# Optimization experiments

Measured on AMD Instinct MI355X. Metric: run time of the kernel, lower is better.

The kernel has to match this reference:

```python
import jax, jax.numpy as jnp
import numpy as np

NQ = 10
C64 = jnp.complex64

# ---- gate matrices (built from traced fp32 params) ----

def u3(t, p, d):
    c = jnp.cos(t * 0.5).astype(C64)
    s = jnp.sin(t * 0.5).astype(C64)
    ep = jnp.exp(1j * p.astype(C64))
    ed = jnp.exp(1j * d.astype(C64))
    return jnp.stack([jnp.stack([c, -ed * s]), jnp.stack([ep * s, ep * ed * c])])

def ry(t):
    c = jnp.cos(t * 0.5).astype(C64)
    s = jnp.sin(t * 0.5).astype(C64)
    return jnp.stack([jnp.stack([c, -s]), jnp.stack([s, c])])

def rz(t):
    e = jnp.exp(-0.5j * t.astype(C64))
    ep = jnp.exp(0.5j * t.astype(C64))
    return jnp.diag(jnp.stack([e, ep]))

def rx(t):
    c = jnp.cos(t * 0.5).astype(C64)
    s = jnp.sin(t * 0.5).astype(C64)
    return jnp.stack([jnp.stack([c, -1j * s]), jnp.stack([-1j * s, c])])

def crz(t):
    one = jnp.ones((), C64)
    return jnp.diag(jnp.stack([one, one, jnp.exp(-0.5j * t.astype(C64)), jnp.exp(0.5j * t.astype(C64))]))

def crx(t):
    return jnp.eye(4, dtype=C64).at[2:, 2:].set(rx(t))

X = jnp.array([[0, 1], [1, 0]], dtype=C64)
CNOT = jnp.array([[1, 0, 0, 0], [0, 1, 0, 0], [0, 0, 0, 1], [0, 0, 1, 0]], dtype=C64)

# ---- gate application on state of shape (B, 2,...,2) ----

def ap1(st, U, w):
    ax = 1 + w
    s = jnp.moveaxis(st, ax, -1)
    s = s @ U.T
    return jnp.moveaxis(s, -1, ax)

def ap2(st, U, a, b):
    s = jnp.moveaxis(st, (1 + a, 1 + b), (-2, -1))
    sh = s.shape
    s = s.reshape(sh[:-2] + (4,)) @ U.T
    return jnp.moveaxis(s.reshape(sh), (-2, -1), (1 + a, 1 + b))

def conv_block(st, w, a, b):
    st = ap1(st, u3(w[0], w[1], w[2]), a)
    st = ap1(st, u3(w[3], w[4], w[5]), b)
    st = ap2(st, CNOT, a, b)
    st = ap1(st, ry(w[6]), a)
    st = ap1(st, rz(w[7]), b)
    st = ap2(st, CNOT, b, a)
    st = ap1(st, ry(w[8]), a)
    st = ap2(st, CNOT, a, b)
    st = ap1(st, u3(w[9], w[10], w[11]), a)
    st = ap1(st, u3(w[12], w[13], w[14]), b)
    return st

def pool_block(st, p, c, t):
    st = ap2(st, crz(p[0]), c, t)
    st = ap1(st, X, c)
    st = ap2(st, crx(p[1]), c, t)
    return st

def zexp(st, w):
    p = jnp.abs(st) ** 2  # fp32
    axes = tuple(ax for ax in range(1, NQ + 1) if ax != 1 + w)
    pz = p.sum(axis=axes)  # (B, 2)
    return pz[:, 0] - pz[:, 1]


def setup_inputs() -> dict:
    key = jax.random.key(0)
    ks = jax.random.split(key, 6)
    two_pi = 2.0 * np.pi
    return {
        "x": jax.random.normal(ks[0], (16384, 1024), dtype=jnp.float32),
        "weights_conv1": jax.random.uniform(ks[1], (10, 15), jnp.float32) * two_pi,
        "weights_conv2": jax.random.uniform(ks[2], (4, 15), jnp.float32) * two_pi,
        "weights_pool1": jax.random.uniform(ks[3], (5, 2), jnp.float32) * two_pi,
        "weights_pool2": jax.random.uniform(ks[4], (2, 2), jnp.float32) * two_pi,
        "weights_fc": jax.random.uniform(ks[5], (3,), jnp.float32) * two_pi,
    }


def reference(x, weights_conv1, weights_conv2, weights_pool1, weights_pool2, weights_fc):
    B = x.shape[0]
    # AmplitudeEmbedding with normalize=True (input already 1024-dim, no padding)
    nrm = jnp.linalg.norm(x, axis=1, keepdims=True)
    st = (x / nrm).astype(C64).reshape((B,) + (2,) * NQ)
    # conv layer 1: even pairs, odd pairs, wraparound (0, 9) reusing row 7
    for i in range(0, NQ, 2):
        st = conv_block(st, weights_conv1[i], i, i + 1)
    for i in range(1, NQ - 1, 2):
        st = conv_block(st, weights_conv1[i], i, i + 1)
    st = conv_block(st, weights_conv1[7], 0, NQ - 1)
    # pool layer 1
    for idx, i in enumerate(range(0, NQ, 2)):
        st = pool_block(st, weights_pool1[idx], i + 1, i)
    # conv layer 2 (stride-2 wires)
    for idx, i in enumerate(range(0, NQ - 2, 2)):
        st = conv_block(st, weights_conv2[idx], i, i + 2)
    # pool layer 2
    for idx, i in enumerate(range(0, NQ - 2, 4)):
        st = pool_block(st, weights_pool2[idx], i + 2, i)
    # fully-connected entanglers + RX rotations
    st = ap2(st, CNOT, 0, 4)
    st = ap2(st, CNOT, 2, 4)
    st = ap2(st, CNOT, 4, 0)
    st = ap1(st, rx(weights_fc[0]), 0)
    st = ap1(st, rx(weights_fc[1]), 2)
    st = ap1(st, rx(weights_fc[2]), 4)
    return jnp.stack([zexp(st, 0), zexp(st, 2)], axis=-1)  # (B, 2)
```

## Files before the change

### kernel.cpp

```cpp
#include <hip/hip_runtime.h>


typedef _Float16 f16;
typedef f16 f16x8 __attribute__((ext_vector_type(8)));
typedef f16 f16x4 __attribute__((ext_vector_type(4)));
typedef f16 f16x2 __attribute__((ext_vector_type(2)));
typedef float f32x4 __attribute__((ext_vector_type(4)));

__device__ inline float2 cmul(float2 a, float2 b) {
    return make_float2(a.x * b.x - a.y * b.y, a.x * b.y + a.y * b.x);
}
__device__ inline float2 cadd(float2 a, float2 b) {
    return make_float2(a.x + b.x, a.y + b.y);
}

struct M2 { float2 m[4]; };

__device__ inline M2 m2_u3(float t, float p, float d) {
    float c = cosf(0.5f * t), s = sinf(0.5f * t);
    float2 ep = make_float2(cosf(p), sinf(p));
    float2 ed = make_float2(cosf(d), sinf(d));
    M2 U;
    U.m[0] = make_float2(c, 0.f);
    U.m[1] = make_float2(-ed.x * s, -ed.y * s);
    U.m[2] = make_float2(ep.x * s, ep.y * s);
    float2 epd = cmul(ep, ed);
    U.m[3] = make_float2(epd.x * c, epd.y * c);
    return U;
}
__device__ inline M2 m2_ry(float t) {
    float c = cosf(0.5f * t), s = sinf(0.5f * t);
    M2 U;
    U.m[0] = make_float2(c, 0.f);  U.m[1] = make_float2(-s, 0.f);
    U.m[2] = make_float2(s, 0.f);  U.m[3] = make_float2(c, 0.f);
    return U;
}
__device__ inline M2 m2_rz(float t) {
    float c = cosf(0.5f * t), s = sinf(0.5f * t);
    M2 U;
    U.m[0] = make_float2(c, -s); U.m[1] = make_float2(0.f, 0.f);
    U.m[2] = make_float2(0.f, 0.f); U.m[3] = make_float2(c, s);
    return U;
}
__device__ inline M2 m2_rx(float t) {
    float c = cosf(0.5f * t), s = sinf(0.5f * t);
    M2 U;
    U.m[0] = make_float2(c, 0.f);   U.m[1] = make_float2(0.f, -s);
    U.m[2] = make_float2(0.f, -s);  U.m[3] = make_float2(c, 0.f);
    return U;
}

__device__ inline void ap2x2(float2& x, float2& y, const M2& U) {
    float2 nx = cadd(cmul(U.m[0], x), cmul(U.m[1], y));
    float2 ny = cadd(cmul(U.m[2], x), cmul(U.m[3], y));
    x = nx; y = ny;
}
__device__ inline void apA(float2 v[4], const M2& U) { ap2x2(v[0], v[2], U); ap2x2(v[1], v[3], U); }
__device__ inline void apB(float2 v[4], const M2& U) { ap2x2(v[0], v[1], U); ap2x2(v[2], v[3], U); }
__device__ inline void swapv(float2& a, float2& b) { float2 t = a; a = b; b = t; }

__device__ inline void conv_col(const float* w, float2 v[4]) {
    apA(v, m2_u3(w[0], w[1], w[2]));
    apB(v, m2_u3(w[3], w[4], w[5]));
    swapv(v[2], v[3]);
    apA(v, m2_ry(w[6]));
    apB(v, m2_rz(w[7]));
    swapv(v[1], v[3]);
    apA(v, m2_ry(w[8]));
    swapv(v[2], v[3]);
    apA(v, m2_u3(w[9], w[10], w[11]));
    apB(v, m2_u3(w[12], w[13], w[14]));
}
__device__ inline void pool_col(const float* p, float2 v[4]) {
    {
        float c = cosf(0.5f * p[0]), s = sinf(0.5f * p[0]);
        v[2] = cmul(v[2], make_float2(c, -s));
        v[3] = cmul(v[3], make_float2(c, s));
    }
    swapv(v[0], v[2]); swapv(v[1], v[3]);
    {
        M2 U = m2_rx(p[1]);
        ap2x2(v[2], v[3], U);
    }
}

__global__ void build_gates(const float* wc1, const float* wc2,
                            const float* wp1, const float* wp2,
                            const float* wfc, int2* gp, float2* gm) {
    const int t = threadIdx.x;
    const int n = t >> 2, c = t & 3;
    if (blockIdx.x != 0 || n >= 27) return;

    float2 v[4];
    for (int i = 0; i < 4; i++) v[i] = make_float2(0.f, 0.f);
    v[c] = make_float2(1.f, 0.f);

    int a, b;
    if (n < 5)        { int i = 2*n;       a = i;   b = i+1; conv_col(wc1 + 15*i, v); }
    else if (n < 9)   { int i = 2*(n-5)+1; a = i;   b = i+1; conv_col(wc1 + 15*i, v); }
    else if (n == 9)  { a = 0; b = 9;      conv_col(wc1 + 105, v); }
    else if (n < 15)  { int idx = n-10, i = 2*idx; a = i+1; b = i; pool_col(wp1 + 2*idx, v); }
    else if (n < 19)  { int idx = n-15, i = 2*idx; a = i; b = i+2; conv_col(wc2 + 15*idx, v); }
    else if (n == 19) { a = 2; b = 0;      pool_col(wp2 + 0, v); }
    else if (n == 20) { a = 6; b = 4;      pool_col(wp2 + 2, v); }
    else if (n <= 23) {
        a = (n == 21) ? 0 : (n == 22) ? 2 : 4;
        b = (n == 23) ? 0 : 4;
        swapv(v[2], v[3]);
    } else {
        a = (n == 24) ? 0 : (n == 25) ? 2 : 4;
        b = a + 1;
        apA(v, m2_rx(wfc[n - 24]));
    }
    if (c == 0) gp[n] = make_int2(9 - a, 9 - b);
    for (int i = 0; i < 4; i++) gm[n * 16 + i * 4 + c] = v[i];
}

#define SIM_BLOCKS 512
#define NORM_BLOCKS 2048

__global__ __launch_bounds__(256) void prep(const float* __restrict__ X,
                                            const int2* __restrict__ gp,
                                            const float2* __restrict__ gm,
                                            float* __restrict__ nrm2,
                                            f16* __restrict__ Xh,
                                            f16* __restrict__ BTh,
                                            float* __restrict__ out) {
    __shared__ float2 st[2][1025];
    const int bid = blockIdx.x;

    if (bid >= SIM_BLOCKS) {
        const int nb = bid - SIM_BLOCKS;
        const int w = threadIdx.x >> 6, l = threadIdx.x & 63;
        if (threadIdx.x < 16) out[nb * 16 + threadIdx.x] = 1.0f;
#pragma unroll
        for (int r = 0; r < 2; r++) {
            const int row = nb * 8 + w * 2 + r;
            const float4* xr = (const float4*)(X + (size_t)row * 1024);
            float s = 0.f;
#pragma unroll
            for (int ch = 0; ch < 4; ch++) {
                float4 v = xr[ch * 64 + l];
                f16x4 h;
                h[0] = (f16)v.x; h[1] = (f16)v.y; h[2] = (f16)v.z; h[3] = (f16)v.w;
                *(f16x4*)(Xh + (size_t)row * 1024 + (ch * 64 + l) * 4) = h;
                s += v.x * v.x + v.y * v.y + v.z * v.z + v.w * v.w;
            }
#pragma unroll
            for (int off = 32; off >= 1; off >>= 1) s += __shfl_xor(s, off, 64);
            if (l == 0) nrm2[row] = s;
        }
        return;
    }

    const int sb = bid;
    const int t0 = (sb & 7) * 128 + (sb >> 3) * 2;

    for (int i = threadIdx.x; i < 1024; i += 256) {
        st[0][i] = make_float2((i == t0) ? 1.f : 0.f, 0.f);
        st[1][i] = make_float2((i == t0 + 1) ? 1.f : 0.f, 0.f);
    }
    __syncthreads();

    for (int g = 0; g < 27; g++) {
        const int2 p = gp[g];
        float2 m[16];
#pragma unroll
        for (int i = 0; i < 16; i++) m[i] = gm[g * 16 + i];
        const int p1 = p.x, p2 = p.y;
        const int lo = min(p1, p2), hi = max(p1, p2);
        const int q = threadIdx.x;
        const int m1 = (1 << lo) - 1;
        int tt = (q & m1) | ((q & ~m1) << 1);
        const int m2m = (1 << hi) - 1;
        const int i0 = (tt & m2m) | ((tt & ~m2m) << 1);
        int idx[4];
        for (int ga = 0; ga < 2; ga++)
            for (int gb = 0; gb < 2; gb++)
                idx[2 * ga + gb] = i0 | (ga << p1) | (gb << p2);
#pragma unroll
        for (int c = 0; c < 2; c++) {
            float2 v[4];
#pragma unroll
            for (int i = 0; i < 4; i++) v[i] = st[c][idx[i]];
#pragma unroll
            for (int i = 0; i < 4; i++) {
                float2 s = make_float2(0.f, 0.f);
#pragma unroll
                for (int j = 0; j < 4; j++) s = cadd(s, cmul(m[i * 4 + j], v[j]));
                st[c][idx[i]] = s;
            }
        }
        __syncthreads();
    }

    for (int s = threadIdx.x; s < 1024; s += 256) {
        const int b9 = (s >> 9) & 1, b7 = (s >> 7) & 1;
        if (b9 | b7) {
            const int grp = b9 ? b7 : 2;
            const int pos = (((s >> 8) & 1) << 7) | (s & 127);
            const int np = grp * 256 + pos;
            f16x2 re, im;
#pragma unroll
            for (int c = 0; c < 2; c++) {
                re[c] = (f16)st[c][s].x;
                im[c] = (f16)st[c][s].y;
            }
            *(f16x2*)(BTh + (size_t)np * 1024 + t0) = re;
            *(f16x2*)(BTh + (size_t)(np + 768) * 1024 + t0) = im;
        }
    }
}

__device__ __forceinline__ void glds16(const void* g, void* l) {
    __builtin_amdgcn_global_load_lds(
        (const __attribute__((address_space(1))) void*)g,
        (__attribute__((address_space(3))) void*)l, 16, 0, 0);
}

__global__ __launch_bounds__(256) void gemm_mfma(const f16* __restrict__ A,
                                                 const f16* __restrict__ Bt,
                                                 const float* __restrict__ nrm2,
                                                 float* __restrict__ out) {
    __shared__ char Ash[16384];
    __shared__ char Bsh[16384];
    const int tid = threadIdx.x;
    const int l = tid & 63, w = tid >> 6;
    const int wr = w >> 1, wc = w & 1;
    const int row0 = blockIdx.x * 128, col0 = blockIdx.y * 128;

    const int srow = l >> 3;
    const int kc = (l & 7) ^ (srow & 7);
    const f16* aS = A  + (size_t)(row0 + 32 * w + srow) * 1024 + kc * 8;
    const f16* bS = Bt + (size_t)(col0 + 32 * w + srow) * 1024 + kc * 8;
    char* aD = Ash + (32 * w) * 128;
    char* bD = Bsh + (32 * w) * 128;

    int aOff[4][2], bOff[4][2];
#pragma unroll
    for (int i = 0; i < 4; i++)
#pragma unroll
        for (int h = 0; h < 2; h++) {
            const int cphys = (((l >> 4) + 4 * h) ^ (l & 7));
            aOff[i][h] = (wr * 64 + i * 16 + (l & 15)) * 128 + cphys * 16;
            bOff[i][h] = (wc * 64 + i * 16 + (l & 15)) * 128 + cphys * 16;
        }

    f32x4 acc[4][4];
    const f32x4 z = {0.f, 0.f, 0.f, 0.f};
#pragma unroll
    for (int i = 0; i < 4; i++)
#pragma unroll
        for (int j = 0; j < 4; j++) acc[i][j] = z;

    for (int k0 = 0; k0 < 1024; k0 += 64) {
#pragma unroll
        for (int g = 0; g < 4; g++) {
            glds16(aS + k0 + g * 8 * 1024, aD + g * 1024);
            glds16(bS + k0 + g * 8 * 1024, bD + g * 1024);
        }
        __syncthreads();
#pragma unroll
        for (int h = 0; h < 2; h++) {
            f16x8 af[4], bf[4];
#pragma unroll
            for (int i = 0; i < 4; i++) {
                af[i] = *(const f16x8*)(Ash + aOff[i][h]);
                bf[i] = *(const f16x8*)(Bsh + bOff[i][h]);
            }
#pragma unroll
            for (int mi = 0; mi < 4; mi++)
#pragma unroll
                for (int ni = 0; ni < 4; ni++)
                    acc[mi][ni] = __builtin_amdgcn_mfma_f32_16x16x32_f16(
                        af[mi], bf[ni], acc[mi][ni], 0, 0, 0);
        }
        __syncthreads();
    }

    float c0[4][4], c1[4][4];
#pragma unroll
    for (int mi = 0; mi < 4; mi++)
#pragma unroll
        for (int rr = 0; rr < 4; rr++) { c0[mi][rr] = 0.f; c1[mi][rr] = 0.f; }
#pragma unroll
    for (int ni = 0; ni < 4; ni++) {
        const int n_glob = col0 + wc * 64 + ni * 16 + (l & 15);
        const int nm = (n_glob >= 768) ? n_glob - 768 : n_glob;
        const int grp = nm >> 8;
        const float w0 = (grp <= 1) ? 1.f : 0.f;
        const float w1 = (grp >= 1) ? 1.f : 0.f;
#pragma unroll
        for (int mi = 0; mi < 4; mi++)
#pragma unroll
            for (int rr = 0; rr < 4; rr++) {
                const float y = acc[mi][ni][rr];
                const float y2 = y * y;
                c0[mi][rr] += w0 * y2;
                c1[mi][rr] += w1 * y2;
            }
    }
#pragma unroll
    for (int off = 1; off < 16; off <<= 1)
#pragma unroll
        for (int mi = 0; mi < 4; mi++)
#pragma unroll
            for (int rr = 0; rr < 4; rr++) {
                c0[mi][rr] += __shfl_xor(c0[mi][rr], off, 64);
                c1[mi][rr] += __shfl_xor(c1[mi][rr], off, 64);
            }
    if ((l & 15) == 0) {
        const int q = l >> 4;
#pragma unroll
        for (int mi = 0; mi < 4; mi++)
#pragma unroll
            for (int rr = 0; rr < 4; rr++) {
                const int row = row0 + wr * 64 + mi * 16 + q * 4 + rr;
                const float inv = -2.0f / nrm2[row];
                atomicAdd(&out[row * 2 + 0], c0[mi][rr] * inv);
                atomicAdd(&out[row * 2 + 1], c1[mi][rr] * inv);
            }
    }
}

extern "C" void kernel_launch(void* const* d_in, const int* in_sizes, int n_in,
                              void* d_out, int out_size, void* d_ws, size_t ws_size,
                              hipStream_t stream) {
    const float* x   = (const float*)d_in[0];
    const float* wc1 = (const float*)d_in[1];
    const float* wc2 = (const float*)d_in[2];
    const float* wp1 = (const float*)d_in[3];
    const float* wp2 = (const float*)d_in[4];
    const float* wfc = (const float*)d_in[5];
    float* out = (float*)d_out;

    uintptr_t wsp = (uintptr_t)d_ws;
    int2*   gp     = (int2*)wsp;
    float2* gm     = (float2*)(wsp + 1024);
    f16*    BTh    = (f16*)(wsp + 8192);
    f16*    Xh     = (f16*)(wsp + 8192 + (3u << 20));
    float*  nrm2   = (float*)(wsp + 8192 + (35u << 20));

    build_gates<<<1, 128, 0, stream>>>(wc1, wc2, wp1, wp2, wfc, gp, gm);
    prep<<<SIM_BLOCKS + NORM_BLOCKS, 256, 0, stream>>>(x, gp, gm, nrm2, Xh, BTh, out);
    gemm_mfma<<<dim3(128, 12), 256, 0, stream>>>(Xh, BTh, nrm2, out);
}
```

Before: 216.3 us.

## Pipeline GEMM with multi-stage LDS buffers and a larger 256x128 block tile

Rewrites the MFMA GEMM main loop as a software pipeline. A is staged through a triple buffer and B through a double buffer in a single 128 KB LDS array, and global-to-LDS loads are issued one or two k-steps ahead. Explicit vmcnt/lgkmcnt waits, s_barrier and setprio keep the MFMA work overlapped with those loads. The block grows to 512 threads covering 256 rows, which halves the grid and reuses each B tile across more rows. The trade-off is much larger LDS use per block, so probably only one block fits per CU despite the launch bound of 2, plus fragile hand-tuned wait counts.

```diff
diff --git a/kernel.cpp b/kernel.cpp
--- a/kernel.cpp
+++ b/kernel.cpp
@@ -218,23 +218,33 @@
         (__attribute__((address_space(3))) void*)l, 16, 0, 0);
 }
 
-__global__ __launch_bounds__(256) void gemm_mfma(const f16* __restrict__ A,
-                                                 const f16* __restrict__ Bt,
-                                                 const float* __restrict__ nrm2,
-                                                 float* __restrict__ out) {
-    __shared__ char Ash[16384];
-    __shared__ char Bsh[16384];
+__global__ __launch_bounds__(512, 2) void gemm_mfma(const f16* __restrict__ A,
+                                                    const f16* __restrict__ Bt,
+                                                    const float* __restrict__ nrm2,
+                                                    float* __restrict__ out) {
+    __shared__ char lds[131072];
     const int tid = threadIdx.x;
     const int l = tid & 63, w = tid >> 6;
     const int wr = w >> 1, wc = w & 1;
-    const int row0 = blockIdx.x * 128, col0 = blockIdx.y * 128;
+    const int row0 = blockIdx.x * 256, col0 = blockIdx.y * 128;
 
     const int srow = l >> 3;
     const int kc = (l & 7) ^ (srow & 7);
     const f16* aS = A  + (size_t)(row0 + 32 * w + srow) * 1024 + kc * 8;
-    const f16* bS = Bt + (size_t)(col0 + 32 * w + srow) * 1024 + kc * 8;
-    char* aD = Ash + (32 * w) * 128;
-    char* bD = Bsh + (32 * w) * 128;
+    const f16* bS = Bt + (size_t)(col0 + 16 * w + srow) * 1024 + kc * 8;
+
+    auto stageA = [&](int t, int p) {
+        char* dst = lds + p * 32768 + (32 * w) * 128;
+#pragma unroll
+        for (int g = 0; g < 4; ++g)
+            glds16(aS + t * 64 + g * 8 * 1024, dst + g * 1024);
+    };
+    auto stageB = [&](int t, int q) {
+        char* dst = lds + 98304 + q * 16384 + (16 * w) * 128;
+#pragma unroll
+        for (int g = 0; g < 2; ++g)
+            glds16(bS + t * 64 + g * 8 * 1024, dst + g * 1024);
+    };
 
     int aOff[4][2], bOff[4][2];
 #pragma unroll
@@ -253,29 +263,64 @@
 #pragma unroll
         for (int j = 0; j < 4; j++) acc[i][j] = z;
 
-    for (int k0 = 0; k0 < 1024; k0 += 64) {
-#pragma unroll
-        for (int g = 0; g < 4; g++) {
-            glds16(aS + k0 + g * 8 * 1024, aD + g * 1024);
-            glds16(bS + k0 + g * 8 * 1024, bD + g * 1024);
-        }
-        __syncthreads();
-#pragma unroll
-        for (int h = 0; h < 2; h++) {
-            f16x8 af[4], bf[4];
-#pragma unroll
-            for (int i = 0; i < 4; i++) {
-                af[i] = *(const f16x8*)(Ash + aOff[i][h]);
-                bf[i] = *(const f16x8*)(Bsh + bOff[i][h]);
-            }
-#pragma unroll
-            for (int mi = 0; mi < 4; mi++)
-#pragma unroll
-                for (int ni = 0; ni < 4; ni++)
-                    acc[mi][ni] = __builtin_amdgcn_mfma_f32_16x16x32_f16(
-                        af[mi], bf[ni], acc[mi][ni], 0, 0, 0);
-        }
-        __syncthreads();
+    stageA(0, 0);
+    stageB(0, 0);
+    stageA(1, 1);
+    asm volatile("s_waitcnt vmcnt(4)" ::: "memory");
+    __builtin_amdgcn_s_barrier();
+    __builtin_amdgcn_sched_barrier(0);
+
+#pragma unroll
+    for (int t = 0; t < 16; ++t) {
+        const char* aB = lds + (t % 3) * 32768;
+        const char* bB = lds + 98304 + (t & 1) * 16384;
+
+        f16x8 af0[4], bf0[4];
+#pragma unroll
+        for (int i = 0; i < 4; i++) {
+            af0[i] = *(const f16x8*)(aB + aOff[i][0]);
+            bf0[i] = *(const f16x8*)(bB + bOff[i][0]);
+        }
+        if (t + 1 < 16) stageB(t + 1, (t + 1) & 1);
+        if (t + 2 < 16) stageA(t + 2, (t + 2) % 3);
+        __builtin_amdgcn_s_barrier();
+        asm volatile("s_waitcnt lgkmcnt(0)" ::: "memory");
+        __builtin_amdgcn_sched_barrier(0);
+        __builtin_amdgcn_s_setprio(1);
+#pragma unroll
+        for (int mi = 0; mi < 4; mi++)
+#pragma unroll
+            for (int ni = 0; ni < 4; ni++)
+                acc[mi][ni] = __builtin_amdgcn_mfma_f32_16x16x32_f16(
+                    af0[mi], bf0[ni], acc[mi][ni], 0, 0, 0);
+        __builtin_amdgcn_sched_barrier(0);
+        __builtin_amdgcn_s_setprio(0);
+        __builtin_amdgcn_s_barrier();
+
+        f16x8 af1[4], bf1[4];
+#pragma unroll
+        for (int i = 0; i < 4; i++) {
+            af1[i] = *(const f16x8*)(aB + aOff[i][1]);
+            bf1[i] = *(const f16x8*)(bB + bOff[i][1]);
+        }
+        __builtin_amdgcn_s_barrier();
+        asm volatile("s_waitcnt lgkmcnt(0)" ::: "memory");
+        __builtin_amdgcn_sched_barrier(0);
+        __builtin_amdgcn_s_setprio(1);
+#pragma unroll
+        for (int mi = 0; mi < 4; mi++)
+#pragma unroll
+            for (int ni = 0; ni < 4; ni++)
+                acc[mi][ni] = __builtin_amdgcn_mfma_f32_16x16x32_f16(
+                    af1[mi], bf1[ni], acc[mi][ni], 0, 0, 0);
+        __builtin_amdgcn_sched_barrier(0);
+        __builtin_amdgcn_s_setprio(0);
+        if (t < 14) {
+            asm volatile("s_waitcnt vmcnt(4)" ::: "memory");
+        } else if (t == 14) {
+            asm volatile("s_waitcnt vmcnt(0)" ::: "memory");
+        }
+        __builtin_amdgcn_s_barrier();
     }
 
     float c0[4][4], c1[4][4];
@@ -343,5 +388,5 @@
 
     build_gates<<<1, 128, 0, stream>>>(wc1, wc2, wp1, wp2, wfc, gp, gm);
     prep<<<SIM_BLOCKS + NORM_BLOCKS, 256, 0, stream>>>(x, gp, gm, nrm2, Xh, BTh, out);
-    gemm_mfma<<<dim3(128, 12), 256, 0, stream>>>(Xh, BTh, nrm2, out);
-}
+    gemm_mfma<<<dim3(64, 12), 512, 0, stream>>>(Xh, BTh, nrm2, out);
+}
```

Result: no change. 217.2 us (+0.5%).

## Enlarge GEMM tiles to 256x256, double-buffer LDS, add XCD-aware block mapping

Applied to the files above, without the earlier changes.

The MFMA GEMM moves from 128x128 tiles with 4 waves to 256x256 tiles with 8 waves. Each wave now computes a 128x64 sub-tile, which raises operand reuse per LDS read. Global-to-LDS loads are double-buffered across a 128KB LDS region, so the next k-slice loads while the current one computes. Only one barrier runs per iteration, and s_setprio raises priority around the MFMA bursts. Blocks are remapped so that row tiles spread across XCDs. The cost is a large register and LDS footprint (one block per CU) and only 384 blocks, which may underfill the GPU.

```diff
diff --git a/kernel.cpp b/kernel.cpp
--- a/kernel.cpp
+++ b/kernel.cpp
@@ -218,69 +218,88 @@
         (__attribute__((address_space(3))) void*)l, 16, 0, 0);
 }
 
-__global__ __launch_bounds__(256) void gemm_mfma(const f16* __restrict__ A,
-                                                 const f16* __restrict__ Bt,
-                                                 const float* __restrict__ nrm2,
-                                                 float* __restrict__ out) {
-    __shared__ char Ash[16384];
-    __shared__ char Bsh[16384];
+__global__ __launch_bounds__(512, 1) void gemm_mfma(const f16* __restrict__ A,
+                                                    const f16* __restrict__ Bt,
+                                                    const float* __restrict__ nrm2,
+                                                    float* __restrict__ out) {
+    __shared__ char lds[131072];
     const int tid = threadIdx.x;
     const int l = tid & 63, w = tid >> 6;
-    const int wr = w >> 1, wc = w & 1;
-    const int row0 = blockIdx.x * 128, col0 = blockIdx.y * 128;
+    const int wr = w >> 2, wc = w & 3;
+
+    const int lin = blockIdx.x;
+    const int xcd = lin & 7;
+    const int mm = lin >> 3;
+    const int rowT = xcd + 8 * (mm / 6);
+    const int j = mm % 6;
+    const int row0 = rowT * 256;
+    const int col0 = j * 256;
 
     const int srow = l >> 3;
     const int kc = (l & 7) ^ (srow & 7);
     const f16* aS = A  + (size_t)(row0 + 32 * w + srow) * 1024 + kc * 8;
     const f16* bS = Bt + (size_t)(col0 + 32 * w + srow) * 1024 + kc * 8;
-    char* aD = Ash + (32 * w) * 128;
-    char* bD = Bsh + (32 * w) * 128;
-
-    int aOff[4][2], bOff[4][2];
-#pragma unroll
-    for (int i = 0; i < 4; i++)
-#pragma unroll
-        for (int h = 0; h < 2; h++) {
-            const int cphys = (((l >> 4) + 4 * h) ^ (l & 7));
-            aOff[i][h] = (wr * 64 + i * 16 + (l & 15)) * 128 + cphys * 16;
+
+    int aOff[8][2], bOff[4][2];
+#pragma unroll
+    for (int h = 0; h < 2; h++) {
+        const int cphys = (((l >> 4) + 4 * h) ^ (l & 7));
+#pragma unroll
+        for (int i = 0; i < 8; i++)
+            aOff[i][h] = (wr * 128 + i * 16 + (l & 15)) * 128 + cphys * 16;
+#pragma unroll
+        for (int i = 0; i < 4; i++)
             bOff[i][h] = (wc * 64 + i * 16 + (l & 15)) * 128 + cphys * 16;
-        }
-
-    f32x4 acc[4][4];
+    }
+
+    f32x4 acc[8][4];
     const f32x4 z = {0.f, 0.f, 0.f, 0.f};
 #pragma unroll
-    for (int i = 0; i < 4; i++)
-#pragma unroll
-        for (int j = 0; j < 4; j++) acc[i][j] = z;
-
-    for (int k0 = 0; k0 < 1024; k0 += 64) {
-#pragma unroll
-        for (int g = 0; g < 4; g++) {
-            glds16(aS + k0 + g * 8 * 1024, aD + g * 1024);
-            glds16(bS + k0 + g * 8 * 1024, bD + g * 1024);
-        }
-        __syncthreads();
-#pragma unroll
-        for (int h = 0; h < 2; h++) {
-            f16x8 af[4], bf[4];
-#pragma unroll
-            for (int i = 0; i < 4; i++) {
-                af[i] = *(const f16x8*)(Ash + aOff[i][h]);
-                bf[i] = *(const f16x8*)(Bsh + bOff[i][h]);
-            }
-#pragma unroll
-            for (int mi = 0; mi < 4; mi++)
+    for (int i = 0; i < 8; i++)
+#pragma unroll
+        for (int n = 0; n < 4; n++) acc[i][n] = z;
+
+    auto stage = [&](int t) {
+        const int b = t & 1;
+        char* aD = lds + b * 32768 + (32 * w) * 128;
+        char* bD = lds + 65536 + b * 32768 + (32 * w) * 128;
+#pragma unroll
+        for (int g = 0; g < 4; ++g) {
+            glds16(aS + t * 64 + g * 8 * 1024, aD + g * 1024);
+            glds16(bS + t * 64 + g * 8 * 1024, bD + g * 1024);
+        }
+    };
+
+    stage(0);
+#pragma unroll 2
+    for (int t = 0; t < 16; ++t) {
+        asm volatile("s_waitcnt vmcnt(0)" ::: "memory");
+        __builtin_amdgcn_s_barrier();
+        if (t + 1 < 16) stage(t + 1);
+
+        const char* aB = lds + (t & 1) * 32768;
+        const char* bB = lds + 65536 + (t & 1) * 32768;
+#pragma unroll
+        for (int h = 0; h < 2; ++h) {
+            f16x8 af[8], bf[4];
+#pragma unroll
+            for (int i = 0; i < 8; i++) af[i] = *(const f16x8*)(aB + aOff[i][h]);
+#pragma unroll
+            for (int i = 0; i < 4; i++) bf[i] = *(const f16x8*)(bB + bOff[i][h]);
+            __builtin_amdgcn_s_setprio(1);
+#pragma unroll
+            for (int mi = 0; mi < 8; mi++)
 #pragma unroll
                 for (int ni = 0; ni < 4; ni++)
                     acc[mi][ni] = __builtin_amdgcn_mfma_f32_16x16x32_f16(
                         af[mi], bf[ni], acc[mi][ni], 0, 0, 0);
-        }
-        __syncthreads();
-    }
-
-    float c0[4][4], c1[4][4];
-#pragma unroll
-    for (int mi = 0; mi < 4; mi++)
+            __builtin_amdgcn_s_setprio(0);
+        }
+    }
+
+    float c0[8][4], c1[8][4];
+#pragma unroll
+    for (int mi = 0; mi < 8; mi++)
 #pragma unroll
         for (int rr = 0; rr < 4; rr++) { c0[mi][rr] = 0.f; c1[mi][rr] = 0.f; }
 #pragma unroll
@@ -291,7 +310,7 @@
         const float w0 = (grp <= 1) ? 1.f : 0.f;
         const float w1 = (grp >= 1) ? 1.f : 0.f;
 #pragma unroll
-        for (int mi = 0; mi < 4; mi++)
+        for (int mi = 0; mi < 8; mi++)
 #pragma unroll
             for (int rr = 0; rr < 4; rr++) {
                 const float y = acc[mi][ni][rr];
@@ -303,19 +322,19 @@
 #pragma unroll
     for (int off = 1; off < 16; off <<= 1)
 #pragma unroll
-        for (int mi = 0; mi < 4; mi++)
+        for (int mi = 0; mi < 8; mi++)
 #pragma unroll
             for (int rr = 0; rr < 4; rr++) {
                 c0[mi][rr] += __shfl_xor(c0[mi][rr], off, 64);
                 c1[mi][rr] += __shfl_xor(c1[mi][rr], off, 64);
             }
     if ((l & 15) == 0) {
-        const int q = l >> 4;
-#pragma unroll
-        for (int mi = 0; mi < 4; mi++)
+        const int q4 = l >> 4;
+#pragma unroll
+        for (int mi = 0; mi < 8; mi++)
 #pragma unroll
             for (int rr = 0; rr < 4; rr++) {
-                const int row = row0 + wr * 64 + mi * 16 + q * 4 + rr;
+                const int row = row0 + wr * 128 + mi * 16 + q4 * 4 + rr;
                 const float inv = -2.0f / nrm2[row];
                 atomicAdd(&out[row * 2 + 0], c0[mi][rr] * inv);
                 atomicAdd(&out[row * 2 + 1], c1[mi][rr] * inv);
@@ -343,5 +362,5 @@
 
     build_gates<<<1, 128, 0, stream>>>(wc1, wc2, wp1, wp2, wfc, gp, gm);
     prep<<<SIM_BLOCKS + NORM_BLOCKS, 256, 0, stream>>>(x, gp, gm, nrm2, Xh, BTh, out);
-    gemm_mfma<<<dim3(128, 12), 256, 0, stream>>>(Xh, BTh, nrm2, out);
-}
+    gemm_mfma<<<384, 512, 0, stream>>>(Xh, BTh, nrm2, out);
+}
```

Measured after the change: 238.7 us. +10.4%, slower.
